# Kernel optimization log

Measured on AMD Instinct MI355X. Metric: run time of the kernel, lower is better.

## Reference

```python
import jax, jax.numpy as jnp
import numpy as np

N = 50000          # nodes
E = 800000         # edges (avg degree 16)
D = 64             # feature dim (in = hidden = out)
L = 3              # GINE layers
BN_EPS = 1e-5
INV_SQRT2 = 1.0 / np.sqrt(2.0)


def setup_inputs() -> dict:
    key = jax.random.key(0)
    ks = jax.random.split(key, 6)
    s = 0.1  # weight scale
    x = jax.random.normal(ks[0], (N, D), jnp.float32)
    edge_index = jax.random.randint(ks[1], (2, E), 0, N)
    edge_attr = jax.random.normal(ks[2], (E, D), jnp.float32)
    W_be = jax.random.normal(ks[3], (D, D), jnp.float32) * s  # shared bond encoder
    b_be = jnp.zeros((D,), jnp.float32)
    eps = jnp.zeros((L,), jnp.float32)          # GINE eps per layer (init 0)
    W1 = jax.random.normal(ks[4], (L, D, D), jnp.float32) * s
    b1 = jnp.zeros((L, D), jnp.float32)
    W2 = jax.random.normal(ks[5], (L, D, D), jnp.float32) * s
    b2 = jnp.zeros((L, D), jnp.float32)
    gamma = jnp.ones((L, D), jnp.float32)
    beta = jnp.zeros((L, D), jnp.float32)
    return dict(x=x, edge_index=edge_index, edge_attr=edge_attr,
                W_be=W_be, b_be=b_be, eps=eps, W1=W1, b1=b1, W2=W2, b2=b2,
                gamma=gamma, beta=beta)


def _gelu(v):
    return jax.nn.gelu(v, approximate=False)  # torch default GELU (erf)


def _bn(h, g, b):
    # BatchNorm1d, training-mode batch statistics (biased variance)
    mu = h.mean(axis=0)
    var = h.var(axis=0)
    return (h - mu) * jax.lax.rsqrt(var + BN_EPS) * g + b


def reference(x, edge_index, edge_attr, W_be, b_be, eps, W1, b1, W2, b2, gamma, beta):
    src, dst = edge_index[0], edge_index[1]  # PyG: row = source j, col = target i
    # Bond encoder is shared across layers and edge_attr is the same each layer,
    # so the embedding is computed once.
    edge_emb = edge_attr @ W_be + b_be  # [E, D]
    for i in range(L):
        m = _gelu(x[src] + edge_emb)                         # edge gather + add + GELU
        agg = jax.ops.segment_sum(m, dst, num_segments=N)    # scatter-add aggregate
        h = (1.0 + eps[i]) * x + agg                         # GINE combine
        h = _gelu(h @ W1[i] + b1[i]) @ W2[i] + b2[i]         # per-layer MLP
        h = _gelu(_bn(h, gamma[i], beta[i]))                 # BN + GELU (dropout p=0)
        x = (x + h) * INV_SQRT2                              # residual (shapes equal)
    return x
```

## Files before the change

### kernel.cpp

```cpp
#include <hip/hip_runtime.h>
#include <hip/hip_bf16.h>
#include <math.h>

#define N_NODES 50000
#define N_EDGES 800000
#define DIM 64
#define NLAYERS 3
#define BN_EPS 1e-5f
#define INV_SQRT2 0.7071067811865475f


__device__ __forceinline__ float gelu_f(float v) {
    return 0.5f * v * (1.0f + erff(v * INV_SQRT2));
}

__device__ __forceinline__ float bf2f(unsigned short u) {
    union { unsigned int i; float f; } t; t.i = ((unsigned int)u) << 16; return t.f;
}
__device__ __forceinline__ unsigned short f2bf(float f) {
    union { float f; unsigned int i; } t; t.f = f;
    unsigned int x = t.i;
    unsigned int r = (x >> 16) & 1u;
    x += 0x7fffu + r;
    return (unsigned short)(x >> 16);
}


__global__ __launch_bounds__(256) void zero_kernel(int* __restrict__ deg) {
    int i = blockIdx.x * 256 + threadIdx.x;
    if (i < N_NODES) deg[i] = 0;
}

__global__ __launch_bounds__(256) void hist_kernel(const int* __restrict__ ei,
                                                   int* __restrict__ deg) {
    int e = blockIdx.x * 256 + threadIdx.x;
    if (e < N_EDGES) atomicAdd(&deg[ei[N_EDGES + e]], 1);
}

__global__ __launch_bounds__(256) void scan_partials(const int* __restrict__ deg,
                                                     int* __restrict__ part) {
    __shared__ int red[256];
    int i = blockIdx.x * 256 + threadIdx.x;
    int v = (i < N_NODES) ? deg[i] : 0;
    red[threadIdx.x] = v; __syncthreads();
    for (int s = 128; s > 0; s >>= 1) {
        if (threadIdx.x < s) red[threadIdx.x] += red[threadIdx.x + s];
        __syncthreads();
    }
    if (threadIdx.x == 0) part[blockIdx.x] = red[0];
}

__global__ __launch_bounds__(256) void scan_top(int* __restrict__ part, int nparts) {
    __shared__ int sh[256];
    int v = (threadIdx.x < nparts) ? part[threadIdx.x] : 0;
    sh[threadIdx.x] = v; __syncthreads();
    for (int s = 1; s < 256; s <<= 1) {
        int t = (threadIdx.x >= s) ? sh[threadIdx.x - s] : 0;
        __syncthreads();
        sh[threadIdx.x] += t;
        __syncthreads();
    }
    if (threadIdx.x < nparts) part[threadIdx.x] = sh[threadIdx.x] - v;
}

__global__ __launch_bounds__(256) void scan_final(const int* __restrict__ deg,
                                                  const int* __restrict__ part,
                                                  int* __restrict__ row_start,
                                                  int* __restrict__ cursor) {
    __shared__ int sh[256];
    int i = blockIdx.x * 256 + threadIdx.x;
    int v = (i < N_NODES) ? deg[i] : 0;
    sh[threadIdx.x] = v; __syncthreads();
    for (int s = 1; s < 256; s <<= 1) {
        int t = (threadIdx.x >= s) ? sh[threadIdx.x - s] : 0;
        __syncthreads();
        sh[threadIdx.x] += t;
        __syncthreads();
    }
    int excl = sh[threadIdx.x] - v + part[blockIdx.x];
    if (i < N_NODES) { row_start[i] = excl; cursor[i] = excl; }
    if (i == N_NODES - 1) row_start[N_NODES] = excl + v;
}

__global__ __launch_bounds__(256) void scatter_kernel(const int* __restrict__ ei,
                                                      int* __restrict__ cursor,
                                                      int* __restrict__ edge_of_pos,
                                                      int* __restrict__ src_sorted) {
    int e = blockIdx.x * 256 + threadIdx.x;
    if (e >= N_EDGES) return;
    int d = ei[N_EDGES + e];
    int pos = atomicAdd(&cursor[d], 1);
    edge_of_pos[pos] = e;
    src_sorted[pos] = ei[e];
}

__global__ __launch_bounds__(256) void be_gemm(const float* __restrict__ attr,
                                               const float* __restrict__ W,
                                               const float* __restrict__ b,
                                               const int* __restrict__ edge_of_pos,
                                               unsigned short* __restrict__ out, int rows) {
    __shared__ float Wl[64][68];
    __shared__ float At[64][132];
    __shared__ int eidl[128];
    int tid = threadIdx.x;
    int row0 = blockIdx.x * 128;
    if (tid < 128) {
        int gr = row0 + tid;
        eidl[tid] = (gr < rows) ? edge_of_pos[gr] : 0;
    }
    {
        const float4* W4 = (const float4*)W;
        for (int i = tid; i < 1024; i += 256) {
            int r = i >> 4, cq = i & 15;
            float4 v = W4[i];
            *(float4*)&Wl[r][cq * 4] = v;
        }
    }
    __syncthreads();
    {
        const float4* attr4 = (const float4*)attr;
        for (int i = tid; i < 2048; i += 256) {
            int r = i >> 4, cq = i & 15;
            int gr = row0 + r;
            float4 v = make_float4(0.f, 0.f, 0.f, 0.f);
            if (gr < rows) v = attr4[(long long)eidl[r] * 16 + cq];
            int c = cq * 4;
            At[c][r] = v.x; At[c + 1][r] = v.y; At[c + 2][r] = v.z; At[c + 3][r] = v.w;
        }
    }
    __syncthreads();
    int cg = tid & 15, rg = tid >> 4;
    int c0 = cg * 4, r0 = rg * 8;
    float acc[8][4];
    float4 bv = *(const float4*)&b[c0];
#pragma unroll
    for (int ri = 0; ri < 8; ri++) {
        acc[ri][0] = bv.x; acc[ri][1] = bv.y; acc[ri][2] = bv.z; acc[ri][3] = bv.w;
    }
    for (int k = 0; k < 64; k++) {
        float4 w = *(float4*)&Wl[k][c0];
        float4 a0 = *(float4*)&At[k][r0];
        float4 a1 = *(float4*)&At[k][r0 + 4];
        float av[8] = {a0.x, a0.y, a0.z, a0.w, a1.x, a1.y, a1.z, a1.w};
#pragma unroll
        for (int ri = 0; ri < 8; ri++) {
            acc[ri][0] += av[ri] * w.x;
            acc[ri][1] += av[ri] * w.y;
            acc[ri][2] += av[ri] * w.z;
            acc[ri][3] += av[ri] * w.w;
        }
    }
#pragma unroll
    for (int ri = 0; ri < 8; ri++) {
        int row = row0 + r0 + ri;
        if (row < rows) {
            ushort4 u;
            u.x = f2bf(acc[ri][0]); u.y = f2bf(acc[ri][1]);
            u.z = f2bf(acc[ri][2]); u.w = f2bf(acc[ri][3]);
            *(ushort4*)(out + (long long)row * DIM + c0) = u;
        }
    }
}

__global__ __launch_bounds__(256) void agg_kernel(const float* __restrict__ x,
                                                  const int* __restrict__ row_start,
                                                  const int* __restrict__ src_sorted,
                                                  const unsigned short* __restrict__ emb,
                                                  const float* __restrict__ eps, int layer,
                                                  float* __restrict__ hout,
                                                  float* __restrict__ stats) {
    if (blockIdx.x == 0 && threadIdx.x < 128) stats[threadIdx.x] = 0.0f;
    int node = (blockIdx.x * 256 + threadIdx.x) >> 6;
    int lane = threadIdx.x & 63;
    if (node >= N_NODES) return;
    int fq = lane & 15;
    int eq = lane >> 4;
    int beg = row_start[node], end = row_start[node + 1];
    const ushort4* emb4 = (const ushort4*)emb;
    const float4* x4 = (const float4*)x;
    float4 acc = make_float4(0.f, 0.f, 0.f, 0.f);
    for (int p0 = beg; p0 < end; p0 += 4) {
        int p = p0 + eq;
        bool valid = (p < end);
        int pc = valid ? p : (end - 1);
        int s = src_sorted[pc];
        ushort4 ev = emb4[(long long)pc * 16 + fq];
        float4 xv = x4[(long long)s * 16 + fq];
        float m0 = gelu_f(xv.x + bf2f(ev.x));
        float m1 = gelu_f(xv.y + bf2f(ev.y));
        float m2 = gelu_f(xv.z + bf2f(ev.z));
        float m3 = gelu_f(xv.w + bf2f(ev.w));
        if (valid) { acc.x += m0; acc.y += m1; acc.z += m2; acc.w += m3; }
    }
    acc.x += __shfl_xor(acc.x, 16, 64); acc.y += __shfl_xor(acc.y, 16, 64);
    acc.z += __shfl_xor(acc.z, 16, 64); acc.w += __shfl_xor(acc.w, 16, 64);
    acc.x += __shfl_xor(acc.x, 32, 64); acc.y += __shfl_xor(acc.y, 32, 64);
    acc.z += __shfl_xor(acc.z, 32, 64); acc.w += __shfl_xor(acc.w, 32, 64);
    if (eq == 0) {
        float e1f = 1.0f + eps[layer];
        float4 xv = x4[(long long)node * 16 + fq];
        float4 o;
        o.x = e1f * xv.x + acc.x; o.y = e1f * xv.y + acc.y;
        o.z = e1f * xv.z + acc.z; o.w = e1f * xv.w + acc.w;
        ((float4*)hout)[(long long)node * 16 + fq] = o;
    }
}

__global__ __launch_bounds__(256) void mlp_kernel(const float* __restrict__ h_in,
                                                  const float* __restrict__ W1,
                                                  const float* __restrict__ b1,
                                                  const float* __restrict__ W2,
                                                  const float* __restrict__ b2,
                                                  float* __restrict__ h2,
                                                  float* __restrict__ stats) {
    __shared__ float W1l[64][68];
    __shared__ float W2l[64][68];
    __shared__ float T[64][68];
    __shared__ float sredS[4][64];
    __shared__ float sredQ[4][64];
    int tid = threadIdx.x;
    int row0 = blockIdx.x * 64;
    {
        const float4* W14 = (const float4*)W1;
        const float4* W24 = (const float4*)W2;
        const float4* h4 = (const float4*)h_in;
        for (int i = tid; i < 1024; i += 256) {
            int r = i >> 4, cq = i & 15;
            *(float4*)&W1l[r][cq * 4] = W14[i];
            *(float4*)&W2l[r][cq * 4] = W24[i];
            int gr = row0 + r;
            float4 v = make_float4(0.f, 0.f, 0.f, 0.f);
            if (gr < N_NODES) v = h4[(long long)gr * 16 + cq];
            int c = cq * 4;
            T[c][r] = v.x; T[c + 1][r] = v.y; T[c + 2][r] = v.z; T[c + 3][r] = v.w;
        }
    }
    __syncthreads();
    int cg = tid & 15, rg = tid >> 4;
    int c0 = cg * 4, r0 = rg * 4;
    float acc[4][4];
    {
        float4 bv = *(const float4*)&b1[c0];
#pragma unroll
        for (int ri = 0; ri < 4; ri++) {
            acc[ri][0] = bv.x; acc[ri][1] = bv.y; acc[ri][2] = bv.z; acc[ri][3] = bv.w;
        }
    }
    for (int k = 0; k < 64; k++) {
        float4 a = *(float4*)&T[k][r0];
        float4 w = *(float4*)&W1l[k][c0];
        float av[4] = {a.x, a.y, a.z, a.w};
#pragma unroll
        for (int ri = 0; ri < 4; ri++) {
            acc[ri][0] += av[ri] * w.x;
            acc[ri][1] += av[ri] * w.y;
            acc[ri][2] += av[ri] * w.z;
            acc[ri][3] += av[ri] * w.w;
        }
    }
    __syncthreads();
#pragma unroll
    for (int ci = 0; ci < 4; ci++) {
        float4 m;
        m.x = gelu_f(acc[0][ci]); m.y = gelu_f(acc[1][ci]);
        m.z = gelu_f(acc[2][ci]); m.w = gelu_f(acc[3][ci]);
        *(float4*)&T[c0 + ci][r0] = m;
    }
    __syncthreads();
    float acc2[4][4];
    {
        float4 bv = *(const float4*)&b2[c0];
#pragma unroll
        for (int ri = 0; ri < 4; ri++) {
            acc2[ri][0] = bv.x; acc2[ri][1] = bv.y; acc2[ri][2] = bv.z; acc2[ri][3] = bv.w;
        }
    }
    for (int k = 0; k < 64; k++) {
        float4 a = *(float4*)&T[k][r0];
        float4 w = *(float4*)&W2l[k][c0];
        float av[4] = {a.x, a.y, a.z, a.w};
#pragma unroll
        for (int ri = 0; ri < 4; ri++) {
            acc2[ri][0] += av[ri] * w.x;
            acc2[ri][1] += av[ri] * w.y;
            acc2[ri][2] += av[ri] * w.z;
            acc2[ri][3] += av[ri] * w.w;
        }
    }
    float4 s = make_float4(0.f, 0.f, 0.f, 0.f);
    float4 q = make_float4(0.f, 0.f, 0.f, 0.f);
#pragma unroll
    for (int ri = 0; ri < 4; ri++) {
        int row = row0 + r0 + ri;
        if (row < N_NODES) {
            float4 o = make_float4(acc2[ri][0], acc2[ri][1], acc2[ri][2], acc2[ri][3]);
            *(float4*)(h2 + (long long)row * DIM + c0) = o;
            s.x += o.x; s.y += o.y; s.z += o.z; s.w += o.w;
            q.x += o.x * o.x; q.y += o.y * o.y; q.z += o.z * o.z; q.w += o.w * o.w;
        }
    }
    s.x += __shfl_xor(s.x, 16, 64); s.y += __shfl_xor(s.y, 16, 64);
    s.z += __shfl_xor(s.z, 16, 64); s.w += __shfl_xor(s.w, 16, 64);
    q.x += __shfl_xor(q.x, 16, 64); q.y += __shfl_xor(q.y, 16, 64);
    q.z += __shfl_xor(q.z, 16, 64); q.w += __shfl_xor(q.w, 16, 64);
    s.x += __shfl_xor(s.x, 32, 64); s.y += __shfl_xor(s.y, 32, 64);
    s.z += __shfl_xor(s.z, 32, 64); s.w += __shfl_xor(s.w, 32, 64);
    q.x += __shfl_xor(q.x, 32, 64); q.y += __shfl_xor(q.y, 32, 64);
    q.z += __shfl_xor(q.z, 32, 64); q.w += __shfl_xor(q.w, 32, 64);
    int wv = tid >> 6;
    if ((tid & 63) < 16) {
        *(float4*)&sredS[wv][c0] = s;
        *(float4*)&sredQ[wv][c0] = q;
    }
    __syncthreads();
    if (tid < 64) {
        float ts = sredS[0][tid] + sredS[1][tid] + sredS[2][tid] + sredS[3][tid];
        float tq = sredQ[0][tid] + sredQ[1][tid] + sredQ[2][tid] + sredQ[3][tid];
        unsafeAtomicAdd(&stats[tid], ts);
        unsafeAtomicAdd(&stats[64 + tid], tq);
    }
}

__global__ __launch_bounds__(256) void bn_kernel(const float* __restrict__ x,
                                                 const float* __restrict__ h2,
                                                 const float* __restrict__ stats,
                                                 const float* __restrict__ gamma,
                                                 const float* __restrict__ beta,
                                                 float* __restrict__ out) {
    int i = blockIdx.x * 256 + threadIdx.x;
    if (i >= N_NODES * DIM / 4) return;
    int f4 = i & 15;
    float4 sum = ((const float4*)stats)[f4];
    float4 sq = ((const float4*)(stats + 64))[f4];
    const float invN = 1.0f / (float)N_NODES;
    float mu0 = sum.x * invN, mu1 = sum.y * invN, mu2 = sum.z * invN, mu3 = sum.w * invN;
    float rs0 = rsqrtf(sq.x * invN - mu0 * mu0 + BN_EPS);
    float rs1 = rsqrtf(sq.y * invN - mu1 * mu1 + BN_EPS);
    float rs2 = rsqrtf(sq.z * invN - mu2 * mu2 + BN_EPS);
    float rs3 = rsqrtf(sq.w * invN - mu3 * mu3 + BN_EPS);
    float4 g = ((const float4*)gamma)[f4];
    float4 bt = ((const float4*)beta)[f4];
    float4 hv = ((const float4*)h2)[i];
    float4 xv = ((const float4*)x)[i];
    float4 o;
    o.x = (xv.x + gelu_f((hv.x - mu0) * rs0 * g.x + bt.x)) * INV_SQRT2;
    o.y = (xv.y + gelu_f((hv.y - mu1) * rs1 * g.y + bt.y)) * INV_SQRT2;
    o.z = (xv.z + gelu_f((hv.z - mu2) * rs2 * g.z + bt.z)) * INV_SQRT2;
    o.w = (xv.w + gelu_f((hv.w - mu3) * rs3 * g.w + bt.w)) * INV_SQRT2;
    ((float4*)out)[i] = o;
}

extern "C" void kernel_launch(void* const* d_in, const int* in_sizes, int n_in,
                              void* d_out, int out_size, void* d_ws, size_t ws_size,
                              hipStream_t stream) {
    const float* x = (const float*)d_in[0];
    const int* ei = (const int*)d_in[1];
    const float* attr = (const float*)d_in[2];
    const float* W_be = (const float*)d_in[3];
    const float* b_be = (const float*)d_in[4];
    const float* eps = (const float*)d_in[5];
    const float* W1 = (const float*)d_in[6];
    const float* b1 = (const float*)d_in[7];
    const float* W2 = (const float*)d_in[8];
    const float* b2 = (const float*)d_in[9];
    const float* gamma = (const float*)d_in[10];
    const float* beta = (const float*)d_in[11];
    float* out = (float*)d_out;

    const size_t emb_bytes = (size_t)N_EDGES * DIM * 2;
    const size_t node_bytes = (size_t)N_NODES * DIM * 4;
    const size_t edge_int_bytes = (size_t)N_EDGES * 4;

    char* ws = (char*)d_ws;
    size_t off = 0;
    auto alloc = [&](size_t bytes) { void* p = ws + off; off += (bytes + 255) & ~(size_t)255; return p; };

    unsigned short* emb = (unsigned short*)alloc(emb_bytes);
    float* aggbuf = (float*)alloc(node_bytes);
    float* h2 = (float*)alloc(node_bytes);
    float* xA = (float*)alloc(node_bytes);
    int* src_sorted = (int*)alloc(edge_int_bytes);
    int* edge_of_pos = (int*)alloc(edge_int_bytes);
    int* row_start = (int*)alloc((size_t)(N_NODES + 1) * 4);
    int* cursor = (int*)alloc((size_t)N_NODES * 4);
    int* deg = (int*)alloc((size_t)N_NODES * 4);
    int* part = (int*)alloc(1024);
    float* stats = (float*)alloc(512);

    const int nodeBlocks = (N_NODES + 255) / 256;
    const int edgeThreadBlocks = (N_EDGES + 255) / 256;
    const int beBlocks = (N_EDGES + 127) / 128;
    const int nodeVecBlocks = (N_NODES * DIM / 4 + 255) / 256;
    const int aggBlocks = (N_NODES + 3) / 4;
    const int mlpBlocks = (N_NODES + 63) / 64;

    zero_kernel<<<nodeBlocks, 256, 0, stream>>>(deg);
    hist_kernel<<<edgeThreadBlocks, 256, 0, stream>>>(ei, deg);
    scan_partials<<<nodeBlocks, 256, 0, stream>>>(deg, part);
    scan_top<<<1, 256, 0, stream>>>(part, nodeBlocks);
    scan_final<<<nodeBlocks, 256, 0, stream>>>(deg, part, row_start, cursor);
    scatter_kernel<<<edgeThreadBlocks, 256, 0, stream>>>(ei, cursor, edge_of_pos, src_sorted);

    be_gemm<<<beBlocks, 256, 0, stream>>>(attr, W_be, b_be, edge_of_pos, emb, N_EDGES);

    for (int l = 0; l < NLAYERS; l++) {
        const float* xin = (l == 0) ? x : ((l == 1) ? xA : out);
        float* xout = (l == 0) ? xA : out;
        agg_kernel<<<aggBlocks, 256, 0, stream>>>(xin, row_start, src_sorted,
                                                  emb, eps, l, aggbuf, stats);
        mlp_kernel<<<mlpBlocks, 256, 0, stream>>>(aggbuf, W1 + l * 4096, b1 + l * 64,
                                                  W2 + l * 4096, b2 + l * 64, h2, stats);
        bn_kernel<<<nodeVecBlocks, 256, 0, stream>>>(xin, h2, stats, gamma + l * 64,
                                                     beta + l * 64, xout);
    }
}
```

Baseline: 763.1 us.

## Use bf16 MFMA for bond-encoder GEMM and share one weight buffer in MLP

The edge bond-encoder GEMM moves from scalar FP32 FMAs to bf16 MFMA 16x16x32 instructions. Inputs and weights are converted to bf16 and stored in LDS in fragment layout. Bounds checks are dropped because E divides evenly by 128. The MLP kernel reuses a single LDS weight buffer for W1 and W2, loading W2 after the first GEMM, which cuts LDS use so more blocks can be resident. Rounding the edge inputs and weights to bf16 lowers precision, and the output stores are now per-element rather than vectorised.

```diff
diff --git a/kernel.cpp b/kernel.cpp
--- a/kernel.cpp
+++ b/kernel.cpp
@@ -8,6 +8,9 @@
 #define NLAYERS 3
 #define BN_EPS 1e-5f
 #define INV_SQRT2 0.7071067811865475f
+
+using f32x4 = __attribute__((ext_vector_type(4))) float;
+using s16x8 = __attribute__((ext_vector_type(8))) short;
 
 
 __device__ __forceinline__ float gelu_f(float v) {
@@ -98,66 +101,71 @@
                                                const float* __restrict__ W,
                                                const float* __restrict__ b,
                                                const int* __restrict__ edge_of_pos,
-                                               unsigned short* __restrict__ out, int rows) {
-    __shared__ float Wl[64][68];
-    __shared__ float At[64][132];
+                                               unsigned short* __restrict__ out) {
+    __shared__ unsigned short fragA[16][64][8];
+    __shared__ unsigned short fragB[8][64][8];
     __shared__ int eidl[128];
     int tid = threadIdx.x;
     int row0 = blockIdx.x * 128;
-    if (tid < 128) {
-        int gr = row0 + tid;
-        eidl[tid] = (gr < rows) ? edge_of_pos[gr] : 0;
-    }
-    {
-        const float4* W4 = (const float4*)W;
-        for (int i = tid; i < 1024; i += 256) {
-            int r = i >> 4, cq = i & 15;
-            float4 v = W4[i];
-            *(float4*)&Wl[r][cq * 4] = v;
-        }
+    if (tid < 128) eidl[tid] = edge_of_pos[row0 + tid];
+    for (int i = tid; i < 1024; i += 256) {
+        int c = i >> 4, k0 = (i & 15) * 4;
+        ushort4 u;
+        u.x = f2bf(W[(k0 + 0) * 64 + c]);
+        u.y = f2bf(W[(k0 + 1) * 64 + c]);
+        u.z = f2bf(W[(k0 + 2) * 64 + c]);
+        u.w = f2bf(W[(k0 + 3) * 64 + c]);
+        int lane = (c & 15) + 16 * ((k0 & 15) >> 2);
+        int j0 = 4 * ((k0 >> 4) & 1);
+        *(ushort4*)&fragB[(c >> 4) * 2 + (k0 >> 5)][lane][j0] = u;
     }
     __syncthreads();
     {
         const float4* attr4 = (const float4*)attr;
         for (int i = tid; i < 2048; i += 256) {
-            int r = i >> 4, cq = i & 15;
-            int gr = row0 + r;
-            float4 v = make_float4(0.f, 0.f, 0.f, 0.f);
-            if (gr < rows) v = attr4[(long long)eidl[r] * 16 + cq];
-            int c = cq * 4;
-            At[c][r] = v.x; At[c + 1][r] = v.y; At[c + 2][r] = v.z; At[c + 3][r] = v.w;
-        }
-    }
-    __syncthreads();
-    int cg = tid & 15, rg = tid >> 4;
-    int c0 = cg * 4, r0 = rg * 8;
-    float acc[8][4];
-    float4 bv = *(const float4*)&b[c0];
-#pragma unroll
-    for (int ri = 0; ri < 8; ri++) {
-        acc[ri][0] = bv.x; acc[ri][1] = bv.y; acc[ri][2] = bv.z; acc[ri][3] = bv.w;
-    }
-    for (int k = 0; k < 64; k++) {
-        float4 w = *(float4*)&Wl[k][c0];
-        float4 a0 = *(float4*)&At[k][r0];
-        float4 a1 = *(float4*)&At[k][r0 + 4];
-        float av[8] = {a0.x, a0.y, a0.z, a0.w, a1.x, a1.y, a1.z, a1.w};
-#pragma unroll
-        for (int ri = 0; ri < 8; ri++) {
-            acc[ri][0] += av[ri] * w.x;
-            acc[ri][1] += av[ri] * w.y;
-            acc[ri][2] += av[ri] * w.z;
-            acc[ri][3] += av[ri] * w.w;
-        }
-    }
-#pragma unroll
-    for (int ri = 0; ri < 8; ri++) {
-        int row = row0 + r0 + ri;
-        if (row < rows) {
+            int r = i >> 4, k0 = (i & 15) * 4;
+            float4 v = attr4[(long long)eidl[r] * 16 + (k0 >> 2)];
             ushort4 u;
-            u.x = f2bf(acc[ri][0]); u.y = f2bf(acc[ri][1]);
-            u.z = f2bf(acc[ri][2]); u.w = f2bf(acc[ri][3]);
-            *(ushort4*)(out + (long long)row * DIM + c0) = u;
+            u.x = f2bf(v.x); u.y = f2bf(v.y); u.z = f2bf(v.z); u.w = f2bf(v.w);
+            int lane = (r & 15) + 16 * ((k0 & 15) >> 2);
+            int j0 = 4 * ((k0 >> 4) & 1);
+            *(ushort4*)&fragA[(r >> 4) * 2 + (k0 >> 5)][lane][j0] = u;
+        }
+    }
+    __syncthreads();
+    int w = tid >> 6, l = tid & 63;
+    s16x8 a[2][2], bf[4][2];
+#pragma unroll
+    for (int mt = 0; mt < 2; mt++)
+#pragma unroll
+        for (int ks = 0; ks < 2; ks++)
+            a[mt][ks] = *(const s16x8*)&fragA[(w * 2 + mt) * 2 + ks][l][0];
+#pragma unroll
+    for (int nt = 0; nt < 4; nt++)
+#pragma unroll
+        for (int ks = 0; ks < 2; ks++)
+            bf[nt][ks] = *(const s16x8*)&fragB[nt * 2 + ks][l][0];
+    f32x4 acc[2][4];
+#pragma unroll
+    for (int mt = 0; mt < 2; mt++)
+#pragma unroll
+        for (int nt = 0; nt < 4; nt++) {
+            f32x4 z = {0.f, 0.f, 0.f, 0.f};
+            z = __builtin_amdgcn_mfma_f32_16x16x32_bf16(a[mt][0], bf[nt][0], z, 0, 0, 0);
+            acc[mt][nt] = __builtin_amdgcn_mfma_f32_16x16x32_bf16(a[mt][1], bf[nt][1], z, 0, 0, 0);
+        }
+    int colbase = l & 15, rowq = 4 * (l >> 4);
+#pragma unroll
+    for (int mt = 0; mt < 2; mt++) {
+        int rbase = row0 + (w * 2 + mt) * 16 + rowq;
+#pragma unroll
+        for (int nt = 0; nt < 4; nt++) {
+            int col = nt * 16 + colbase;
+            float bias = b[col];
+#pragma unroll
+            for (int i = 0; i < 4; i++) {
+                out[(long long)(rbase + i) * DIM + col] = f2bf(acc[mt][nt][i] + bias);
+            }
         }
     }
 }
@@ -213,8 +221,7 @@
                                                   const float* __restrict__ b2,
                                                   float* __restrict__ h2,
                                                   float* __restrict__ stats) {
-    __shared__ float W1l[64][68];
-    __shared__ float W2l[64][68];
+    __shared__ float Wl[64][68];
     __shared__ float T[64][68];
     __shared__ float sredS[4][64];
     __shared__ float sredQ[4][64];
@@ -222,12 +229,10 @@
     int row0 = blockIdx.x * 64;
     {
         const float4* W14 = (const float4*)W1;
-        const float4* W24 = (const float4*)W2;
         const float4* h4 = (const float4*)h_in;
         for (int i = tid; i < 1024; i += 256) {
             int r = i >> 4, cq = i & 15;
-            *(float4*)&W1l[r][cq * 4] = W14[i];
-            *(float4*)&W2l[r][cq * 4] = W24[i];
+            *(float4*)&Wl[r][cq * 4] = W14[i];
             int gr = row0 + r;
             float4 v = make_float4(0.f, 0.f, 0.f, 0.f);
             if (gr < N_NODES) v = h4[(long long)gr * 16 + cq];
@@ -248,7 +253,7 @@
     }
     for (int k = 0; k < 64; k++) {
         float4 a = *(float4*)&T[k][r0];
-        float4 w = *(float4*)&W1l[k][c0];
+        float4 w = *(float4*)&Wl[k][c0];
         float av[4] = {a.x, a.y, a.z, a.w};
 #pragma unroll
         for (int ri = 0; ri < 4; ri++) {
@@ -266,6 +271,13 @@
         m.z = gelu_f(acc[2][ci]); m.w = gelu_f(acc[3][ci]);
         *(float4*)&T[c0 + ci][r0] = m;
     }
+    {
+        const float4* W24 = (const float4*)W2;
+        for (int i = tid; i < 1024; i += 256) {
+            int r = i >> 4, cq = i & 15;
+            *(float4*)&Wl[r][cq * 4] = W24[i];
+        }
+    }
     __syncthreads();
     float acc2[4][4];
     {
@@ -277,7 +289,7 @@
     }
     for (int k = 0; k < 64; k++) {
         float4 a = *(float4*)&T[k][r0];
-        float4 w = *(float4*)&W2l[k][c0];
+        float4 w = *(float4*)&Wl[k][c0];
         float av[4] = {a.x, a.y, a.z, a.w};
 #pragma unroll
         for (int ri = 0; ri < 4; ri++) {
@@ -389,7 +401,7 @@
 
     const int nodeBlocks = (N_NODES + 255) / 256;
     const int edgeThreadBlocks = (N_EDGES + 255) / 256;
-    const int beBlocks = (N_EDGES + 127) / 128;
+    const int beBlocks = N_EDGES / 128;
     const int nodeVecBlocks = (N_NODES * DIM / 4 + 255) / 256;
     const int aggBlocks = (N_NODES + 3) / 4;
     const int mlpBlocks = (N_NODES + 63) / 64;
@@ -401,7 +413,7 @@
     scan_final<<<nodeBlocks, 256, 0, stream>>>(deg, part, row_start, cursor);
     scatter_kernel<<<edgeThreadBlocks, 256, 0, stream>>>(ei, cursor, edge_of_pos, src_sorted);
 
-    be_gemm<<<beBlocks, 256, 0, stream>>>(attr, W_be, b_be, edge_of_pos, emb, N_EDGES);
+    be_gemm<<<beBlocks, 256, 0, stream>>>(attr, W_be, b_be, edge_of_pos, emb);
 
     for (int l = 0; l < NLAYERS; l++) {
         const float* xin = (l == 0) ? x : ((l == 1) ? xA : out);
```

New measurement: 748.0 us. 1.02x faster.
